# Kernel optimization log

Measured on AMD Instinct MI355X. Metric: run time of the kernel, lower is better.

The kernel has to match this reference:

```python
import jax, jax.numpy as jnp
import numpy as np

WEIGHT0 = 1.0
WEIGHT1 = 1.0
GAMMA = 2.0
N = 33554432  # number of flattened per-pixel predictions
EPS = 1e-6    # keep probabilities strictly inside (0,1) so log is finite


def setup_inputs() -> dict:
    key = jax.random.key(0)
    k1, k2 = jax.random.split(key)
    u = jax.random.uniform(k1, (N,), dtype=jnp.float32)
    inp = u * (1.0 - 2.0 * EPS) + EPS  # probabilities in (eps, 1-eps)
    tgt = jax.random.randint(k2, (N,), 0, 2, dtype=jnp.int32)
    return {"input": inp, "target": tgt}


def reference(input, target):
    # Faithful vectorized form of the per-element Python loop:
    #   t==1: log(p)   * |1-p|^gamma * w1
    #   else: log(1-p) * |p|^gamma   * w0
    # summed, negated, divided by N.
    pos = jnp.log(input) * jnp.abs(1.0 - input) ** GAMMA * WEIGHT1
    neg = jnp.log(1.0 - input) * jnp.abs(input) ** GAMMA * WEIGHT0
    per_el = jnp.where(target == 1, pos, neg)
    return -jnp.mean(per_el)
```

## Files before the change

### kernel.cpp

```cpp
#include <hip/hip_runtime.h>


typedef float v4f __attribute__((ext_vector_type(4)));
typedef int   v4i __attribute__((ext_vector_type(4)));

constexpr int   N_TOTAL   = 33554432;
constexpr int   N_VEC     = N_TOTAL / 4;
constexpr int   THREADS   = 256;
constexpr int   BLOCKS    = 2048;
constexpr int   GTHREADS  = BLOCKS * THREADS;
constexpr int   STEPS     = N_VEC / GTHREADS;
constexpr float NEG_INV_N = -1.0f / 33554432.0f;

__device__ __forceinline__ float term4(v4f p, v4i t) {
    float r = 0.0f;
#pragma unroll
    for (int j = 0; j < 4; ++j) {
        float s = (t[j] == 1) ? p[j] : (1.0f - p[j]);
        float q = 1.0f - s;
        r += __logf(s) * q * q;
    }
    return r;
}

__global__ __launch_bounds__(THREADS) void focal_partial_kernel(
    const v4f* __restrict__ inp,
    const v4i* __restrict__ tgt,
    float* __restrict__ partials)
{
    const int gtid = blockIdx.x * THREADS + threadIdx.x;

    float acc = 0.0f;
#pragma unroll
    for (int k = 0; k < STEPS; ++k) {
        const int idx = gtid + k * GTHREADS;
        v4f p = inp[idx];
        v4i t = tgt[idx];
        acc += term4(p, t);
    }

#pragma unroll
    for (int off = 32; off > 0; off >>= 1)
        acc += __shfl_down(acc, off, 64);

    __shared__ float ws[THREADS / 64];
    int lane = threadIdx.x & 63;
    int wave = threadIdx.x >> 6;
    if (lane == 0) ws[wave] = acc;
    __syncthreads();

    if (threadIdx.x == 0)
        partials[blockIdx.x] = ws[0] + ws[1] + ws[2] + ws[3];
}

__global__ __launch_bounds__(THREADS) void focal_final_kernel(
    const float* __restrict__ partials,
    float* __restrict__ out)
{
    float acc = 0.0f;
#pragma unroll
    for (int k = 0; k < BLOCKS / THREADS; ++k)
        acc += partials[k * THREADS + threadIdx.x];

#pragma unroll
    for (int off = 32; off > 0; off >>= 1)
        acc += __shfl_down(acc, off, 64);

    __shared__ float ws[THREADS / 64];
    int lane = threadIdx.x & 63;
    int wave = threadIdx.x >> 6;
    if (lane == 0) ws[wave] = acc;
    __syncthreads();

    if (threadIdx.x == 0)
        out[0] = (ws[0] + ws[1] + ws[2] + ws[3]) * NEG_INV_N;
}

extern "C" void kernel_launch(void* const* d_in, const int* in_sizes, int n_in,
                              void* d_out, int out_size, void* d_ws, size_t ws_size,
                              hipStream_t stream) {
    const v4f* inp = (const v4f*)d_in[0];
    const v4i* tgt = (const v4i*)d_in[1];
    float*     out = (float*)d_out;
    float*     partials = (float*)d_ws;

    focal_partial_kernel<<<BLOCKS, THREADS, 0, stream>>>(inp, tgt, partials);
    focal_final_kernel<<<1, THREADS, 0, stream>>>(partials, out);
}
```

Before: 273.7 us.

## Stream inputs through LDS with direct global-to-LDS async loads pipeline

Replaces direct register loads with per-wave global_load_lds 16-byte transfers into an 8-deep LDS ring buffer. Manual vmcnt waits keep several loads in flight while earlier stages are computed. The block count drops from 2048 to 512, so each wave handles more steps. The aim is more memory-level parallelism and hidden load latency for this bandwidth-bound reduction. In exchange it uses LDS, hand-counted waitcnts that must match the compiler's other memory ops, and a tail that assumes STEPS mod DEPTH alignment.

```diff
diff --git a/kernel.cpp b/kernel.cpp
--- a/kernel.cpp
+++ b/kernel.cpp
@@ -7,10 +7,19 @@
 constexpr int   N_TOTAL   = 33554432;
 constexpr int   N_VEC     = N_TOTAL / 4;
 constexpr int   THREADS   = 256;
-constexpr int   BLOCKS    = 2048;
-constexpr int   GTHREADS  = BLOCKS * THREADS;
-constexpr int   STEPS     = N_VEC / GTHREADS;
+constexpr int   WAVES     = THREADS / 64;
+constexpr int   BLOCKS    = 512;
+constexpr int   GWAVES    = BLOCKS * WAVES;
+constexpr int   STEPS     = N_VEC / (GWAVES * 64);
+constexpr int   DEPTH     = 8;
 constexpr float NEG_INV_N = -1.0f / 33554432.0f;
+
+__device__ __forceinline__ void gload_lds16(const void* g, void* l) {
+    __builtin_amdgcn_global_load_lds(
+        (const __attribute__((address_space(1))) unsigned int*)g,
+        (__attribute__((address_space(3))) unsigned int*)l,
+        16, 0, 0);
+}
 
 __device__ __forceinline__ float term4(v4f p, v4i t) {
     float r = 0.0f;
@@ -23,29 +32,57 @@
     return r;
 }
 
+#define WAITVM(N) asm volatile("s_waitcnt vmcnt(" #N ")" ::: "memory")
+
 __global__ __launch_bounds__(THREADS) void focal_partial_kernel(
     const v4f* __restrict__ inp,
     const v4i* __restrict__ tgt,
     float* __restrict__ partials)
 {
-    const int gtid = blockIdx.x * THREADS + threadIdx.x;
+    __shared__ v4f ldsP[WAVES][DEPTH][64];
+    __shared__ v4i ldsT[WAVES][DEPTH][64];
+
+    const int lane = threadIdx.x & 63;
+    const int wave = threadIdx.x >> 6;
+    const int gw   = blockIdx.x * WAVES + wave;
+
+#define STAGE(d, s) do {                                   \
+        const int _v = ((s) * GWAVES + gw) * 64 + lane;    \
+        gload_lds16(&inp[_v], &ldsP[wave][(d)][0]);        \
+        gload_lds16(&tgt[_v], &ldsT[wave][(d)][0]);        \
+    } while (0)
+
+#define COMPUTE(b) do {                                    \
+        v4f _p = ldsP[wave][(b)][lane];                    \
+        v4i _t = ldsT[wave][(b)][lane];                    \
+        acc += term4(_p, _t);                              \
+    } while (0)
+
+#pragma unroll
+    for (int d = 0; d < DEPTH - 1; ++d)
+        STAGE(d, d);
 
     float acc = 0.0f;
-#pragma unroll
-    for (int k = 0; k < STEPS; ++k) {
-        const int idx = gtid + k * GTHREADS;
-        v4f p = inp[idx];
-        v4i t = tgt[idx];
-        acc += term4(p, t);
+
+    for (int s = 0; s < STEPS - DEPTH + 1; ++s) {
+        STAGE((s + DEPTH - 1) & (DEPTH - 1), s + DEPTH - 1);
+        WAITVM(14);
+        COMPUTE(s & (DEPTH - 1));
     }
+
+    WAITVM(12); COMPUTE(1);
+    WAITVM(10); COMPUTE(2);
+    WAITVM(8);  COMPUTE(3);
+    WAITVM(6);  COMPUTE(4);
+    WAITVM(4);  COMPUTE(5);
+    WAITVM(2);  COMPUTE(6);
+    WAITVM(0);  COMPUTE(7);
 
 #pragma unroll
     for (int off = 32; off > 0; off >>= 1)
         acc += __shfl_down(acc, off, 64);
 
-    __shared__ float ws[THREADS / 64];
-    int lane = threadIdx.x & 63;
-    int wave = threadIdx.x >> 6;
+    __shared__ float ws[WAVES];
     if (lane == 0) ws[wave] = acc;
     __syncthreads();
 
```

After: 274.4 us. No clear change (+0.2%).
